# Performance work log

Measured on AMD Instinct MI355X. Metric: run time of the kernel, lower is better.

Reference implementation:

```python
import jax, jax.numpy as jnp
import numpy as np

S = 8          # nodes per subgraph (last node is the anchor)
B = 8192       # number of subgraphs in the batch
N = B * S      # total nodes
E_PER = S * S  # edges per subgraph (dense local connectivity)
DIN, DOUT = 512, 256
EPS = 1e-12


def _block_edges(key):
    # local src/dst in [0,S) per subgraph, offset to global node ids
    k1, k2 = jax.random.split(key)
    src = jax.random.randint(k1, (B, E_PER), 0, S)
    dst = jax.random.randint(k2, (B, E_PER), 0, S)
    off = (jnp.arange(B) * S)[:, None]
    return (src + off).reshape(-1), (dst + off).reshape(-1)


def setup_inputs() -> dict:
    key = jax.random.key(0)
    ks = jax.random.split(key, 10)
    pos_src, pos_dst = _block_edges(ks[0])
    neg_src, neg_dst = _block_edges(ks[1])
    return {
        "pos_x": jax.random.normal(ks[2], (N, DIN), jnp.float32),
        "neg_x": jax.random.normal(ks[3], (N, DIN), jnp.float32),
        "pos_src": pos_src, "pos_dst": pos_dst,
        "pos_w": jax.random.uniform(ks[4], (B * E_PER,), jnp.float32),
        "neg_src": neg_src, "neg_dst": neg_dst,
        "neg_w": jax.random.uniform(ks[5], (B * E_PER,), jnp.float32),
        "W_gcn": jax.random.normal(ks[6], (DIN, DOUT), jnp.float32) / np.sqrt(DIN),
        "b_gcn": jnp.zeros((DOUT,), jnp.float32),
        "prelu_a": jnp.float32(0.25),
        "W_bil": jax.random.normal(ks[7], (DOUT, DOUT), jnp.float32) / np.sqrt(DOUT),
        "b_bil": jnp.zeros((1,), jnp.float32),
    }


def _l2norm(x):
    return x / jnp.maximum(jnp.linalg.norm(x, axis=1, keepdims=True), EPS)


def _gcn_branch(x, src, dst, w, W_gcn, b_gcn, prelu_a):
    # GraphConv(norm='none') with edge weights: h = A_w (X W) + b
    xw = x @ W_gcn                                      # [N, DOUT]
    agg = jnp.zeros_like(xw).at[dst].add(w[:, None] * xw[src])
    h = agg + b_gcn
    h = jnp.where(h >= 0, h, prelu_a * h)               # PReLU (single param)
    h = h.reshape(B, S, -1)                             # fixed-size subgraphs
    pool = jnp.mean(h[:, :-1], axis=1)                  # mean over non-anchor nodes
    anchor = h[:, -1]                                   # last node per subgraph
    return _l2norm(pool), _l2norm(anchor)


def reference(pos_x, neg_x, pos_src, pos_dst, pos_w, neg_src, neg_dst, neg_w,
              W_gcn, b_gcn, prelu_a, W_bil, b_bil):
    pos_pool, anchor = _gcn_branch(pos_x, pos_src, pos_dst, pos_w, W_gcn, b_gcn, prelu_a)
    neg_pool, _ = _gcn_branch(neg_x, neg_src, neg_dst, neg_w, W_gcn, b_gcn, prelu_a)
    # Bilinear(D, D, 1): score_b = pool_b^T W anchor_b + bias
    pos_scores = jnp.einsum('bd,de,be->b', pos_pool, W_bil, anchor) + b_bil[0]
    neg_scores = jnp.einsum('bd,de,be->b', neg_pool, W_bil, anchor) + b_bil[0]
    return pos_scores, neg_scores
```

## Files before the change

### kernel.cpp

```cpp
#include <hip/hip_runtime.h>
#include <math.h>

#define SS 8
#define NBLK 8192
#define DIN 512
#define DOUT 256
#define GB 8
#define MT 64
#define BK 32
#define KSTEPS 16
#define VSTR 264
#define EPSN 1e-12f

typedef __bf16 bf16;
typedef __bf16 bf16x8 __attribute__((ext_vector_type(8)));
typedef float  f32x4  __attribute__((ext_vector_type(4)));

__global__ void prep_kernel(const float* __restrict__ W_gcn,
                            const float* __restrict__ W_bil,
                            bf16* __restrict__ Wt,
                            bf16* __restrict__ Wh,
                            bf16* __restrict__ Wl) {
    int idx = blockIdx.x * 256 + threadIdx.x;
    if (idx < DIN * DOUT) {
        int k = idx >> 8, n = idx & 255;
        Wt[n * DIN + k] = (bf16)W_gcn[idx];
    } else {
        int j = idx - DIN * DOUT;
        float wv = W_bil[j];
        bf16 h = (bf16)wv;
        Wh[j] = h;
        Wl[j] = (bf16)(wv - (float)h);
    }
}

__global__ __launch_bounds__(256, 2) void cola_fused3(
    const float* __restrict__ pos_x, const float* __restrict__ neg_x,
    const int* __restrict__ pos_src, const int* __restrict__ pos_dst,
    const float* __restrict__ pos_w,
    const int* __restrict__ neg_src, const int* __restrict__ neg_dst,
    const float* __restrict__ neg_w,
    const bf16* __restrict__ Wt, const bf16* __restrict__ Wh,
    const bf16* __restrict__ Wl,
    const float* __restrict__ b_gcn, const float* __restrict__ prelu_a,
    const float* __restrict__ b_bil, float* __restrict__ out)
{
    __shared__ bf16  AsP[MT * BK];
    __shared__ bf16  AsN[MT * BK];
    __shared__ bf16  Bs[DOUT * BK];
    __shared__ float pool_pos[GB * DOUT];
    __shared__ float v_lds[GB * DOUT];
    __shared__ bf16  ahs[GB * VSTR];
    __shared__ bf16  als[GB * VSTR];
    __shared__ float adjP[GB][SS][SS];
    __shared__ float adjN[GB][SS][SS];
    __shared__ float red[5 * GB];

    const int t    = threadIdx.x;
    const int wg   = blockIdx.x;
    const int w    = t >> 6;
    const int lane = t & 63;
    const int q    = lane >> 4;
    const int r15  = lane & 15;

    for (int i = t; i < GB * 64; i += 256) { ((float*)adjP)[i] = 0.f; ((float*)adjN)[i] = 0.f; }
    if (t < 5 * GB) red[t] = 0.f;
    __syncthreads();

    {
        int2   sp2 = ((const int2*)pos_src)[wg * 256 + t];
        int2   dp2 = ((const int2*)pos_dst)[wg * 256 + t];
        float2 wp2 = ((const float2*)pos_w)[wg * 256 + t];
        int2   sn2 = ((const int2*)neg_src)[wg * 256 + t];
        int2   dn2 = ((const int2*)neg_dst)[wg * 256 + t];
        float2 wn2 = ((const float2*)neg_w)[wg * 256 + t];
        int gl = t >> 5;
        int base = (wg * GB + gl) * SS;
        atomicAdd(&adjP[gl][dp2.x - base][sp2.x - base], wp2.x);
        atomicAdd(&adjP[gl][dp2.y - base][sp2.y - base], wp2.y);
        atomicAdd(&adjN[gl][dn2.x - base][sn2.x - base], wn2.x);
        atomicAdd(&adjN[gl][dn2.y - base][sn2.y - base], wn2.y);
    }

    f32x4 accp[4][4], accn[4][4];
#pragma unroll
    for (int mi = 0; mi < 4; ++mi)
#pragma unroll
        for (int ni = 0; ni < 4; ++ni) {
            accp[mi][ni] = (f32x4){0.f, 0.f, 0.f, 0.f};
            accn[mi][ni] = (f32x4){0.f, 0.f, 0.f, 0.f};
        }

    const int arow = t >> 2;
    const int akc  = (t & 3) * 8;
    const float* app = pos_x + (size_t)(wg * MT + arow) * DIN + akc;
    const float* anp = neg_x + (size_t)(wg * MT + arow) * DIN + akc;
    const bf16*  bp  = Wt + (size_t)t * DIN;
    const int trot = (t >> 1) & 3;

    float4 pa0 = *(const float4*)(app);
    float4 pa1 = *(const float4*)(app + 4);
    float4 na0 = *(const float4*)(anp);
    float4 na1 = *(const float4*)(anp + 4);
    bf16x8 bv0 = *(const bf16x8*)(bp + 0);
    bf16x8 bv1 = *(const bf16x8*)(bp + 8);
    bf16x8 bv2 = *(const bf16x8*)(bp + 16);
    bf16x8 bv3 = *(const bf16x8*)(bp + 24);

    bf16* awP = AsP + arow * BK + akc;
    bf16* awN = AsN + arow * BK + akc;
    bf16* bw  = Bs + t * BK;

    for (int s = 0; s < KSTEPS; ++s) {
        bf16x8 av;
        av[0] = (bf16)pa0.x; av[1] = (bf16)pa0.y; av[2] = (bf16)pa0.z; av[3] = (bf16)pa0.w;
        av[4] = (bf16)pa1.x; av[5] = (bf16)pa1.y; av[6] = (bf16)pa1.z; av[7] = (bf16)pa1.w;
        *(bf16x8*)awP = av;
        av[0] = (bf16)na0.x; av[1] = (bf16)na0.y; av[2] = (bf16)na0.z; av[3] = (bf16)na0.w;
        av[4] = (bf16)na1.x; av[5] = (bf16)na1.y; av[6] = (bf16)na1.z; av[7] = (bf16)na1.w;
        *(bf16x8*)awN = av;
        *(bf16x8*)(bw + (((0 + trot) & 3) << 3)) = bv0;
        *(bf16x8*)(bw + (((1 + trot) & 3) << 3)) = bv1;
        *(bf16x8*)(bw + (((2 + trot) & 3) << 3)) = bv2;
        *(bf16x8*)(bw + (((3 + trot) & 3) << 3)) = bv3;
        __syncthreads();

        if (s < KSTEPS - 1) {
            pa0 = *(const float4*)(app + (s + 1) * BK);
            pa1 = *(const float4*)(app + (s + 1) * BK + 4);
            na0 = *(const float4*)(anp + (s + 1) * BK);
            na1 = *(const float4*)(anp + (s + 1) * BK + 4);
            bv0 = *(const bf16x8*)(bp + (s + 1) * BK + 0);
            bv1 = *(const bf16x8*)(bp + (s + 1) * BK + 8);
            bv2 = *(const bf16x8*)(bp + (s + 1) * BK + 16);
            bv3 = *(const bf16x8*)(bp + (s + 1) * BK + 24);
        }

        bf16x8 afp[4], afn[4], bfv[4];
#pragma unroll
        for (int mi = 0; mi < 4; ++mi) {
            afp[mi] = *(const bf16x8*)(AsP + (mi * 16 + r15) * BK + q * 8);
            afn[mi] = *(const bf16x8*)(AsN + (mi * 16 + r15) * BK + q * 8);
        }
#pragma unroll
        for (int ni = 0; ni < 4; ++ni) {
            int n = w * 64 + ni * 16 + r15;
            int slot = (q + ((n >> 1) & 3)) & 3;
            bfv[ni] = *(const bf16x8*)(Bs + n * BK + slot * 8);
        }
#pragma unroll
        for (int mi = 0; mi < 4; ++mi)
#pragma unroll
            for (int ni = 0; ni < 4; ++ni) {
                accp[mi][ni] = __builtin_amdgcn_mfma_f32_16x16x32_bf16(
                    afp[mi], bfv[ni], accp[mi][ni], 0, 0, 0);
                accn[mi][ni] = __builtin_amdgcn_mfma_f32_16x16x32_bf16(
                    afn[mi], bfv[ni], accn[mi][ni], 0, 0, 0);
            }
        __syncthreads();
    }

    const float pa = *prelu_a;

#pragma unroll
    for (int mi = 0; mi < 4; ++mi) {
        const int gl = mi * 2 + (q >> 1);
        float part = 0.f;
#pragma unroll
        for (int ni = 0; ni < 4; ++ni) {
            float r0, r1, r2, r3, r4, r5, r6, r7;
#pragma unroll
            for (int r = 0; r < 4; ++r) {
                float own = accp[mi][ni][r];
                float oth = __shfl_xor(own, 16);
                float lo = ((q & 1) == 0) ? own : oth;
                float hi = ((q & 1) == 0) ? oth : own;
                if (r == 0) { r0 = lo; r4 = hi; }
                else if (r == 1) { r1 = lo; r5 = hi; }
                else if (r == 2) { r2 = lo; r6 = hi; }
                else            { r3 = lo; r7 = hi; }
            }
            int c = w * 64 + ni * 16 + r15;
            float bg = b_gcn[c];
            float pool = 0.f, anch = 0.f;
#pragma unroll
            for (int d = 0; d < 8; ++d) {
                const float* ar = &adjP[gl][d][0];
                float a = bg + ar[0]*r0 + ar[1]*r1 + ar[2]*r2 + ar[3]*r3
                             + ar[4]*r4 + ar[5]*r5 + ar[6]*r6 + ar[7]*r7;
                float h = (a >= 0.f) ? a : pa * a;
                if (d < 7) pool += h; else anch = h;
            }
            float pl = pool * (1.f / 7.f);
            if ((q & 1) == 0) {
                pool_pos[gl * DOUT + c] = pl;
                part += pl * pl;
            } else {
                bf16 hh = (bf16)anch;
                ahs[gl * VSTR + c] = hh;
                als[gl * VSTR + c] = (bf16)(anch - (float)hh);
                part += anch * anch;
            }
        }
        part += __shfl_xor(part, 8);
        part += __shfl_xor(part, 4);
        part += __shfl_xor(part, 2);
        part += __shfl_xor(part, 1);
        if (r15 == 0) atomicAdd((q & 1) ? &red[GB + gl] : &red[gl], part);
    }
    __syncthreads();

    {
        f32x4 accv[4];
#pragma unroll
        for (int ni = 0; ni < 4; ++ni) accv[ni] = (f32x4){0.f, 0.f, 0.f, 0.f};
        const int ga = (r15 & 7) * VSTR;
#pragma unroll
        for (int ks = 0; ks < 8; ++ks) {
            bf16x8 ah_f = *(const bf16x8*)(ahs + ga + ks * 32 + q * 8);
            bf16x8 al_f = *(const bf16x8*)(als + ga + ks * 32 + q * 8);
#pragma unroll
            for (int ni = 0; ni < 4; ++ni) {
                int d = w * 64 + ni * 16 + r15;
                bf16x8 bh = *(const bf16x8*)(Wh + (size_t)d * DOUT + ks * 32 + q * 8);
                bf16x8 bl = *(const bf16x8*)(Wl + (size_t)d * DOUT + ks * 32 + q * 8);
                accv[ni] = __builtin_amdgcn_mfma_f32_16x16x32_bf16(ah_f, bh, accv[ni], 0, 0, 0);
                accv[ni] = __builtin_amdgcn_mfma_f32_16x16x32_bf16(al_f, bh, accv[ni], 0, 0, 0);
                accv[ni] = __builtin_amdgcn_mfma_f32_16x16x32_bf16(ah_f, bl, accv[ni], 0, 0, 0);
            }
        }
        float sp[4] = {0.f, 0.f, 0.f, 0.f};
        if (q < 2) {
#pragma unroll
            for (int ni = 0; ni < 4; ++ni) {
                int c = w * 64 + ni * 16 + r15;
#pragma unroll
                for (int r = 0; r < 4; ++r) {
                    int g = q * 4 + r;
                    v_lds[g * DOUT + c] = accv[ni][r];
                    sp[r] += accv[ni][r] * pool_pos[g * DOUT + c];
                }
            }
        }
#pragma unroll
        for (int r = 0; r < 4; ++r) {
            sp[r] += __shfl_xor(sp[r], 8);
            sp[r] += __shfl_xor(sp[r], 4);
            sp[r] += __shfl_xor(sp[r], 2);
            sp[r] += __shfl_xor(sp[r], 1);
        }
        if (q < 2 && r15 == 0) {
#pragma unroll
            for (int r = 0; r < 4; ++r) atomicAdd(&red[3 * GB + q * 4 + r], sp[r]);
        }
    }
    __syncthreads();

#pragma unroll
    for (int mi = 0; mi < 4; ++mi) {
        const int gl = mi * 2 + (q >> 1);
        float part = 0.f;
#pragma unroll
        for (int ni = 0; ni < 4; ++ni) {
            float r0, r1, r2, r3, r4, r5, r6, r7;
#pragma unroll
            for (int r = 0; r < 4; ++r) {
                float own = accn[mi][ni][r];
                float oth = __shfl_xor(own, 16);
                float lo = ((q & 1) == 0) ? own : oth;
                float hi = ((q & 1) == 0) ? oth : own;
                if (r == 0) { r0 = lo; r4 = hi; }
                else if (r == 1) { r1 = lo; r5 = hi; }
                else if (r == 2) { r2 = lo; r6 = hi; }
                else            { r3 = lo; r7 = hi; }
            }
            int c = w * 64 + ni * 16 + r15;
            float bg = b_gcn[c];
            float pool = 0.f;
#pragma unroll
            for (int d = 0; d < 7; ++d) {
                const float* ar = &adjN[gl][d][0];
                float a = bg + ar[0]*r0 + ar[1]*r1 + ar[2]*r2 + ar[3]*r3
                             + ar[4]*r4 + ar[5]*r5 + ar[6]*r6 + ar[7]*r7;
                float h = (a >= 0.f) ? a : pa * a;
                pool += h;
            }
            float pl = pool * (1.f / 7.f);
            part += ((q & 1) == 0) ? pl * v_lds[gl * DOUT + c] : pl * pl;
        }
        part += __shfl_xor(part, 8);
        part += __shfl_xor(part, 4);
        part += __shfl_xor(part, 2);
        part += __shfl_xor(part, 1);
        if (r15 == 0) atomicAdd((q & 1) ? &red[2 * GB + gl] : &red[4 * GB + gl], part);
    }
    __syncthreads();

    if (t < GB) {
        float np = fmaxf(sqrtf(red[t]), EPSN);
        float na = fmaxf(sqrtf(red[GB + t]), EPSN);
        float nn = fmaxf(sqrtf(red[2 * GB + t]), EPSN);
        float bb = b_bil[0];
        out[wg * GB + t]        = red[3 * GB + t] / (np * na) + bb;
        out[NBLK + wg * GB + t] = red[4 * GB + t] / (nn * na) + bb;
    }
}

extern "C" void kernel_launch(void* const* d_in, const int* in_sizes, int n_in,
                              void* d_out, int out_size, void* d_ws, size_t ws_size,
                              hipStream_t stream) {
    const float* pos_x   = (const float*)d_in[0];
    const float* neg_x   = (const float*)d_in[1];
    const int*   pos_src = (const int*)d_in[2];
    const int*   pos_dst = (const int*)d_in[3];
    const float* pos_w   = (const float*)d_in[4];
    const int*   neg_src = (const int*)d_in[5];
    const int*   neg_dst = (const int*)d_in[6];
    const float* neg_w   = (const float*)d_in[7];
    const float* W_gcn   = (const float*)d_in[8];
    const float* b_gcn   = (const float*)d_in[9];
    const float* prelu_a = (const float*)d_in[10];
    const float* W_bil   = (const float*)d_in[11];
    const float* b_bil   = (const float*)d_in[12];
    float* outp = (float*)d_out;

    bf16* Wt = (bf16*)d_ws;
    bf16* Wh = Wt + DIN * DOUT;
    bf16* Wl = Wh + DOUT * DOUT;

    prep_kernel<<<(DIN * DOUT + DOUT * DOUT) / 256, 256, 0, stream>>>(W_gcn, W_bil, Wt, Wh, Wl);
    cola_fused3<<<NBLK / GB, 256, 0, stream>>>(
        pos_x, neg_x, pos_src, pos_dst, pos_w, neg_src, neg_dst, neg_w,
        Wt, Wh, Wl, b_gcn, prelu_a, b_bil, outp);
}
```

Baseline: 367.0 us.

## Stream GEMM tiles into double-buffered LDS via direct global-to-LDS loads

After: 360.3 us. Within noise of the previous version (-1.8%).

```diff
diff --git a/kernel.cpp b/kernel.cpp
--- a/kernel.cpp
+++ b/kernel.cpp
@@ -1,4 +1,5 @@
 #include <hip/hip_runtime.h>
+#include <stdint.h>
 #include <math.h>
 
 #define SS 8
@@ -15,6 +16,20 @@
 typedef __bf16 bf16;
 typedef __bf16 bf16x8 __attribute__((ext_vector_type(8)));
 typedef float  f32x4  __attribute__((ext_vector_type(4)));
+
+typedef __attribute__((address_space(3))) uint32_t       lds_u32;
+typedef __attribute__((address_space(1))) const uint32_t g_u32;
+
+__device__ __forceinline__ void dma16(const void* g, void* l) {
+    __builtin_amdgcn_global_load_lds((g_u32*)g, (lds_u32*)l, 16, 0, 0);
+}
+
+__device__ __forceinline__ bf16x8 cvt8(f32x4 lo, f32x4 hi) {
+    bf16x8 r;
+    r[0] = (bf16)lo[0]; r[1] = (bf16)lo[1]; r[2] = (bf16)lo[2]; r[3] = (bf16)lo[3];
+    r[4] = (bf16)hi[0]; r[5] = (bf16)hi[1]; r[6] = (bf16)hi[2]; r[7] = (bf16)hi[3];
+    return r;
+}
 
 __global__ void prep_kernel(const float* __restrict__ W_gcn,
                             const float* __restrict__ W_bil,
@@ -34,7 +49,7 @@
     }
 }
 
-__global__ __launch_bounds__(256, 2) void cola_fused3(
+__global__ __launch_bounds__(256, 2) void cola_fused4(
     const float* __restrict__ pos_x, const float* __restrict__ neg_x,
     const int* __restrict__ pos_src, const int* __restrict__ pos_dst,
     const float* __restrict__ pos_w,
@@ -45,16 +60,16 @@
     const float* __restrict__ b_gcn, const float* __restrict__ prelu_a,
     const float* __restrict__ b_bil, float* __restrict__ out)
 {
-    __shared__ bf16  AsP[MT * BK];
-    __shared__ bf16  AsN[MT * BK];
-    __shared__ bf16  Bs[DOUT * BK];
-    __shared__ float pool_pos[GB * DOUT];
-    __shared__ float v_lds[GB * DOUT];
-    __shared__ bf16  ahs[GB * VSTR];
-    __shared__ bf16  als[GB * VSTR];
+    __shared__ __align__(16) float bufA[2][2][MT * BK];
+    __shared__ __align__(16) bf16  bufB[2][DOUT * BK];
     __shared__ float adjP[GB][SS][SS];
     __shared__ float adjN[GB][SS][SS];
     __shared__ float red[5 * GB];
+
+    float* pool_pos = (float*)&bufB[0][0];
+    float* v_lds    = pool_pos + GB * DOUT;
+    bf16*  ahs      = (bf16*)(v_lds + GB * DOUT);
+    bf16*  als      = ahs + GB * VSTR;
 
     const int t    = threadIdx.x;
     const int wg   = blockIdx.x;
@@ -62,6 +77,7 @@
     const int lane = t & 63;
     const int q    = lane >> 4;
     const int r15  = lane & 15;
+    const int row0 = wg * MT;
 
     for (int i = t; i < GB * 64; i += 256) { ((float*)adjP)[i] = 0.f; ((float*)adjN)[i] = 0.f; }
     if (t < 5 * GB) red[t] = 0.f;
@@ -82,6 +98,30 @@
         atomicAdd(&adjN[gl][dn2.y - base][sn2.y - base], wn2.y);
     }
 
+    const int arow_off = lane >> 3;
+    const int akq      = (lane & 7) ^ arow_off;
+    const int bn_off = lane >> 2;
+    const int bkq    = lane & 3;
+
+    auto issue = [&](int s, int bufi) {
+        const int kbase = s * BK;
+#pragma unroll
+        for (int h = 0; h < 2; ++h) {
+            int c = w * 2 + h;
+            int row = c * 8 + arow_off;
+            dma16(pos_x + (size_t)(row0 + row) * DIN + kbase + akq * 4,
+                  &bufA[bufi][0][c * 256]);
+            dma16(neg_x + (size_t)(row0 + row) * DIN + kbase + akq * 4,
+                  &bufA[bufi][1][c * 256]);
+        }
+#pragma unroll
+        for (int j = 0; j < 4; ++j) {
+            int c = w * 4 + j;
+            dma16(Wt + (size_t)(c * 16 + bn_off) * DIN + kbase + bkq * 8,
+                  &bufB[bufi][c * 512]);
+        }
+    };
+
     f32x4 accp[4][4], accn[4][4];
 #pragma unroll
     for (int mi = 0; mi < 4; ++mi)
@@ -91,62 +131,29 @@
             accn[mi][ni] = (f32x4){0.f, 0.f, 0.f, 0.f};
         }
 
-    const int arow = t >> 2;
-    const int akc  = (t & 3) * 8;
-    const float* app = pos_x + (size_t)(wg * MT + arow) * DIN + akc;
-    const float* anp = neg_x + (size_t)(wg * MT + arow) * DIN + akc;
-    const bf16*  bp  = Wt + (size_t)t * DIN;
-    const int trot = (t >> 1) & 3;
-
-    float4 pa0 = *(const float4*)(app);
-    float4 pa1 = *(const float4*)(app + 4);
-    float4 na0 = *(const float4*)(anp);
-    float4 na1 = *(const float4*)(anp + 4);
-    bf16x8 bv0 = *(const bf16x8*)(bp + 0);
-    bf16x8 bv1 = *(const bf16x8*)(bp + 8);
-    bf16x8 bv2 = *(const bf16x8*)(bp + 16);
-    bf16x8 bv3 = *(const bf16x8*)(bp + 24);
-
-    bf16* awP = AsP + arow * BK + akc;
-    bf16* awN = AsN + arow * BK + akc;
-    bf16* bw  = Bs + t * BK;
-
+    issue(0, 0);
+    int cur = 0;
     for (int s = 0; s < KSTEPS; ++s) {
-        bf16x8 av;
-        av[0] = (bf16)pa0.x; av[1] = (bf16)pa0.y; av[2] = (bf16)pa0.z; av[3] = (bf16)pa0.w;
-        av[4] = (bf16)pa1.x; av[5] = (bf16)pa1.y; av[6] = (bf16)pa1.z; av[7] = (bf16)pa1.w;
-        *(bf16x8*)awP = av;
-        av[0] = (bf16)na0.x; av[1] = (bf16)na0.y; av[2] = (bf16)na0.z; av[3] = (bf16)na0.w;
-        av[4] = (bf16)na1.x; av[5] = (bf16)na1.y; av[6] = (bf16)na1.z; av[7] = (bf16)na1.w;
-        *(bf16x8*)awN = av;
-        *(bf16x8*)(bw + (((0 + trot) & 3) << 3)) = bv0;
-        *(bf16x8*)(bw + (((1 + trot) & 3) << 3)) = bv1;
-        *(bf16x8*)(bw + (((2 + trot) & 3) << 3)) = bv2;
-        *(bf16x8*)(bw + (((3 + trot) & 3) << 3)) = bv3;
         __syncthreads();
-
-        if (s < KSTEPS - 1) {
-            pa0 = *(const float4*)(app + (s + 1) * BK);
-            pa1 = *(const float4*)(app + (s + 1) * BK + 4);
-            na0 = *(const float4*)(anp + (s + 1) * BK);
-            na1 = *(const float4*)(anp + (s + 1) * BK + 4);
-            bv0 = *(const bf16x8*)(bp + (s + 1) * BK + 0);
-            bv1 = *(const bf16x8*)(bp + (s + 1) * BK + 8);
-            bv2 = *(const bf16x8*)(bp + (s + 1) * BK + 16);
-            bv3 = *(const bf16x8*)(bp + (s + 1) * BK + 24);
-        }
+        if (s + 1 < KSTEPS) issue(s + 1, cur ^ 1);
 
         bf16x8 afp[4], afn[4], bfv[4];
+        const int q0 = (2 * q) ^ (r15 & 7);
+        const int q1 = q0 ^ 1;
 #pragma unroll
         for (int mi = 0; mi < 4; ++mi) {
-            afp[mi] = *(const bf16x8*)(AsP + (mi * 16 + r15) * BK + q * 8);
-            afn[mi] = *(const bf16x8*)(AsN + (mi * 16 + r15) * BK + q * 8);
+            int m = mi * 16 + r15;
+            f32x4 lo = *(const f32x4*)&bufA[cur][0][m * BK + q0 * 4];
+            f32x4 hi = *(const f32x4*)&bufA[cur][0][m * BK + q1 * 4];
+            afp[mi] = cvt8(lo, hi);
+            lo = *(const f32x4*)&bufA[cur][1][m * BK + q0 * 4];
+            hi = *(const f32x4*)&bufA[cur][1][m * BK + q1 * 4];
+            afn[mi] = cvt8(lo, hi);
         }
 #pragma unroll
         for (int ni = 0; ni < 4; ++ni) {
             int n = w * 64 + ni * 16 + r15;
-            int slot = (q + ((n >> 1) & 3)) & 3;
-            bfv[ni] = *(const bf16x8*)(Bs + n * BK + slot * 8);
+            bfv[ni] = *(const bf16x8*)&bufB[cur][n * BK + q * 8];
         }
 #pragma unroll
         for (int mi = 0; mi < 4; ++mi)
@@ -157,8 +164,9 @@
                 accn[mi][ni] = __builtin_amdgcn_mfma_f32_16x16x32_bf16(
                     afn[mi], bfv[ni], accn[mi][ni], 0, 0, 0);
             }
-        __syncthreads();
-    }
+        cur ^= 1;
+    }
+    __syncthreads();
 
     const float pa = *prelu_a;
 
@@ -329,7 +337,7 @@
     bf16* Wl = Wh + DOUT * DOUT;
 
     prep_kernel<<<(DIN * DOUT + DOUT * DOUT) / 256, 256, 0, stream>>>(W_gcn, W_bil, Wt, Wh, Wl);
-    cola_fused3<<<NBLK / GB, 256, 0, stream>>>(
+    cola_fused4<<<NBLK / GB, 256, 0, stream>>>(
         pos_x, neg_x, pos_src, pos_dst, pos_w, neg_src, neg_dst, neg_w,
         Wt, Wh, Wl, b_gcn, prelu_a, b_bil, outp);
 }
```
